# Optimization experiments

Hardware: AMD Instinct MI355X
Metric: run time of the kernel (lower is better)

## Reference

```python
import jax, jax.numpy as jnp
import numpy as np

D_MODEL = 2048
N_HEAD = 32
N_KV_HEAD = 8
HEAD_DIM = D_MODEL // N_HEAD  # 64
N_REP = N_HEAD // N_KV_HEAD   # 4
B, T = 2, 2048


def setup_inputs() -> dict:
    key = jax.random.key(0)
    ks = jax.random.split(key, 5)
    s = 0.02
    return {
        "x": jax.random.normal(ks[0], (B, T, D_MODEL), dtype=jnp.float32),
        "Wq": jax.random.normal(ks[1], (D_MODEL, N_HEAD * HEAD_DIM), dtype=jnp.float32) * s,
        "Wk": jax.random.normal(ks[2], (D_MODEL, N_KV_HEAD * HEAD_DIM), dtype=jnp.float32) * s,
        "Wv": jax.random.normal(ks[3], (D_MODEL, N_KV_HEAD * HEAD_DIM), dtype=jnp.float32) * s,
        "Wo": jax.random.normal(ks[4], (N_HEAD * HEAD_DIM, D_MODEL), dtype=jnp.float32) * s,
        "mask": 1,
    }


def _rope_tables(t_len, dim, dtype):
    inv_freq = 1.0 / (10000.0 ** (jnp.arange(0, dim, 2, dtype=jnp.float32) / dim))
    freqs = jnp.arange(t_len, dtype=jnp.float32)[:, None] * inv_freq[None, :]  # [T, dim/2]
    return jnp.cos(freqs).astype(dtype), jnp.sin(freqs).astype(dtype)


def _apply_rope(x, cos, sin):
    # x: [B, H, T, D]; cos/sin: [T, D/2]; half-concat layout as in source
    x1, x2 = x[..., ::2], x[..., 1::2]
    return jnp.concatenate([x1 * cos - x2 * sin, x1 * sin + x2 * cos], axis=-1)


def reference(x, Wq, Wk, Wv, Wo, mask):
    b, t, c = x.shape
    q = (x @ Wq).reshape(b, t, N_HEAD, HEAD_DIM).transpose(0, 2, 1, 3)      # [B,H,T,D]
    k = (x @ Wk).reshape(b, t, N_KV_HEAD, HEAD_DIM).transpose(0, 2, 1, 3)   # [B,Hkv,T,D]
    v = (x @ Wv).reshape(b, t, N_KV_HEAD, HEAD_DIM).transpose(0, 2, 1, 3)
    cos, sin = _rope_tables(t, HEAD_DIM, x.dtype)
    q = _apply_rope(q, cos, sin)
    k = _apply_rope(k, cos, sin)
    k = jnp.repeat(k, N_REP, axis=1)  # [B,H,T,D]
    v = jnp.repeat(v, N_REP, axis=1)
    scale = 1.0 / np.sqrt(HEAD_DIM)
    scores = jnp.einsum('bhtd,bhsd->bhts', q, k) * scale  # [B,H,T,T]
    if mask:
        causal = jnp.tril(jnp.ones((t, t), dtype=bool))
        scores = jnp.where(causal, scores, jnp.float32(-jnp.inf).astype(scores.dtype))
    weights = jax.nn.softmax(scores, axis=-1)
    out = jnp.einsum('bhts,bhsd->bhtd', weights, v)        # [B,H,T,D]
    out = out.transpose(0, 2, 1, 3).reshape(b, t, c)
    return out @ Wo
```

## Files before the change

### kernel.cpp

```cpp
#include <hip/hip_runtime.h>
#include <stdint.h>

#define D_MODEL 2048
#define N_HEAD 32
#define N_KV_HEAD 8
#define HEAD_DIM 64
#define BATCH 2
#define SEQ 2048
#define ROWS (BATCH*SEQ)
#define QKV_N 3072
#define SCL2F 0.18033688011112042f

typedef __attribute__((ext_vector_type(4))) float f32x4;
typedef __attribute__((ext_vector_type(8))) short bf16x8;

__device__ __forceinline__ float bflo(unsigned u){ return __uint_as_float(u << 16); }
__device__ __forceinline__ float bfhi(unsigned u){ return __uint_as_float(u & 0xFFFF0000u); }
__device__ __forceinline__ unsigned f2bf(float f){
  unsigned u = __float_as_uint(f);
  u += 0x7FFFu + ((u >> 16) & 1u);
  return u >> 16;
}
__device__ __forceinline__ unsigned cvtpk(float a, float b){
  unsigned r;
  asm("v_cvt_pk_bf16_f32 %0, %1, %2" : "=v"(r) : "v"(a), "v"(b));
  return r;
}

__device__ __forceinline__ void async_copy16(const void* g, void* lds){
  __builtin_amdgcn_global_load_lds(
      (const __attribute__((address_space(1))) void*)g,
      (__attribute__((address_space(3))) void*)lds, 16, 0, 0);
}

__global__ __launch_bounds__(256) void k_prep(const float* __restrict__ x,
                                              const float* __restrict__ Wq,
                                              const float* __restrict__ Wk,
                                              const float* __restrict__ Wv,
                                              const float* __restrict__ Wo,
                                              unsigned short* __restrict__ xb,
                                              unsigned short* __restrict__ Wqkvt,
                                              unsigned short* __restrict__ Wot,
                                              float* __restrict__ ct,
                                              float* __restrict__ st){
  __shared__ float tile[64][65];
  const int bid = blockIdx.x;
  const int tid = threadIdx.x;
  if (bid < 8192) {
    int i = bid*256 + tid;
    float4 v = ((const float4*)x)[i];
    unsigned lo = f2bf(v.x) | (f2bf(v.y) << 16);
    unsigned hi = f2bf(v.z) | (f2bf(v.w) << 16);
    ((uint2*)xb)[i] = make_uint2(lo, hi);
    return;
  }
  if (bid < 10752) {
    const int rel0 = bid - 8192;
    const float* W; unsigned short* Wt; int N; int rel;
    if (rel0 < 1024)      { W = Wq; Wt = Wqkvt;                         N = 2048; rel = rel0; }
    else if (rel0 < 1280) { W = Wk; Wt = Wqkvt + (size_t)2048*D_MODEL;  N = 512;  rel = rel0 - 1024; }
    else if (rel0 < 1536) { W = Wv; Wt = Wqkvt + (size_t)2560*D_MODEL;  N = 512;  rel = rel0 - 1280; }
    else                  { W = Wo; Wt = Wot;                           N = 2048; rel = rel0 - 1536; }
    const int ntn = N >> 6;
    const int tk = rel / ntn, tn = rel % ntn;
    #pragma unroll
    for (int i = 0; i < 4; ++i) {
      int idx4 = tid + 256*i;
      int r = idx4 >> 4;
      int c4 = idx4 & 15;
      float4 v = *(const float4*)(W + (size_t)(tk*64 + r)*N + tn*64 + c4*4);
      tile[r][c4*4+0] = v.x; tile[r][c4*4+1] = v.y;
      tile[r][c4*4+2] = v.z; tile[r][c4*4+3] = v.w;
    }
    __syncthreads();
    #pragma unroll
    for (int i = 0; i < 8; ++i) {
      int o2 = tid + 256*i;
      int n  = o2 >> 5;
      int k2 = o2 & 31;
      unsigned lo = f2bf(tile[k2*2+0][n]);
      unsigned hi = f2bf(tile[k2*2+1][n]);
      *(unsigned*)(Wt + (size_t)(tn*64 + n)*D_MODEL + tk*64 + k2*2) = lo | (hi << 16);
    }
    return;
  }
  {
    int gid = (bid - 10752)*256 + tid;
    int t = gid >> 5, d = gid & 31;
    float inv = exp2f(-13.287712379549449f * ((float)d * (1.0f/32.0f)));
    float a = (float)t * inv;
    ct[gid] = cosf(a);
    st[gid] = sinf(a);
  }
}

__global__ __launch_bounds__(256) void k_kv_prep(unsigned short* __restrict__ QKVb,
                                                 unsigned short* __restrict__ Vt,
                                                 const float* __restrict__ ct,
                                                 const float* __restrict__ st){
  __shared__ __align__(16) unsigned short tl[64*64];
  const int bid = blockIdx.x;
  const int tid = threadIdx.x;
  if (bid < 128) {
    int gid = bid*256 + tid;
    int row = gid >> 3;
    int h = gid & 7;
    int t = row & (SEQ-1);
    unsigned* p = (unsigned*)(QKVb + (size_t)row*QKV_N + 2048 + h*HEAD_DIM);
    float o1[32], o2[32];
    #pragma unroll
    for (int d = 0; d < 32; ++d) {
      unsigned u = p[d];
      float x1 = bflo(u), x2 = bfhi(u);
      float c = ct[t*32+d], s = st[t*32+d];
      o1[d] = x1*c - x2*s;
      o2[d] = x1*s + x2*c;
    }
    #pragma unroll
    for (int i = 0; i < 16; ++i) {
      p[i]    = f2bf(o1[2*i]) | (f2bf(o1[2*i+1]) << 16);
      p[16+i] = f2bf(o2[2*i]) | (f2bf(o2[2*i+1]) << 16);
    }
    return;
  }
  const int rel = bid - 128;
  const int bk = rel >> 5;
  const int stt = rel & 31;
  const int b = bk >> 3, kvh = bk & 7;
  #pragma unroll
  for (int it = 0; it < 2; ++it) {
    int i = tid + 256*it;
    int s = i >> 3, c = i & 7;
    uint4 v = *(const uint4*)(QKVb + (size_t)(b*SEQ + stt*64 + s)*QKV_N + 2560 + kvh*HEAD_DIM + c*8);
    *(uint4*)(tl + s*64 + ((c ^ (s&7))*8)) = v;
  }
  __syncthreads();
  const int d = tid & 63;
  const int w = tid >> 6;
  #pragma unroll
  for (int it = 0; it < 2; ++it) {
    int seg = w + it*4;
    unsigned short tmp[8];
    #pragma unroll
    for (int k = 0; k < 8; ++k) {
      int s = seg*8 + k;
      tmp[k] = tl[s*64 + (((d>>3) ^ (s&7))*8) + (d&7)];
    }
    *(uint4*)(Vt + ((size_t)bk*64 + d)*SEQ + stt*64 + seg*8) = *(uint4*)tmp;
  }
}

template<typename OUT_T>
__global__ __launch_bounds__(256) void k_gemm_bt(const unsigned short* __restrict__ A,
                                                 const unsigned short* __restrict__ Bt,
                                                 OUT_T* __restrict__ C,
                                                 int M, int N, int K){
  __shared__ unsigned short As[128*32];
  __shared__ unsigned short Bs[128*32];
  const int nbn = N >> 7;
  const int bswz = ((int)blockIdx.x & 7)*((int)gridDim.x >> 3) + ((int)blockIdx.x >> 3);
  const int bm = bswz / nbn, bn = bswz % nbn;
  const int m0 = bm << 7, n0 = bn << 7;
  const int tid = threadIdx.x;
  const int wid = tid >> 6, lane = tid & 63;
  const int wr = wid >> 1, wc = wid & 1;

  f32x4 acc[4][4] = {};

  const int ldr = lane >> 2;
  const int ldc = (lane & 3) * 8;
  const int fr  = lane & 15;
  const int fk  = (lane >> 4) * 8;

  for (int k0 = 0; k0 < K; k0 += 32) {
    #pragma unroll
    for (int i = 0; i < 2; ++i) {
      int chunk = wid*2 + i;
      int row = chunk*16 + ldr;
      async_copy16(A  + (size_t)(m0+row)*K + k0 + ldc, (void*)(As + chunk*512));
      async_copy16(Bt + (size_t)(n0+row)*K + k0 + ldc, (void*)(Bs + chunk*512));
    }
    __syncthreads();
    bf16x8 a[4], b[4];
    #pragma unroll
    for (int m = 0; m < 4; ++m) a[m] = *(const bf16x8*)(As + (wr*64 + m*16 + fr)*32 + fk);
    #pragma unroll
    for (int n = 0; n < 4; ++n) b[n] = *(const bf16x8*)(Bs + (wc*64 + n*16 + fr)*32 + fk);
    #pragma unroll
    for (int m = 0; m < 4; ++m)
      #pragma unroll
      for (int n = 0; n < 4; ++n)
        acc[m][n] = __builtin_amdgcn_mfma_f32_16x16x32_bf16(a[m], b[n], acc[m][n], 0, 0, 0);
    __syncthreads();
  }

  const int crow = (lane >> 4) * 4, ccol = lane & 15;
  #pragma unroll
  for (int m = 0; m < 4; ++m){
    #pragma unroll
    for (int n = 0; n < 4; ++n){
      size_t base = (size_t)(m0 + wr*64 + m*16 + crow)*N + (n0 + wc*64 + n*16 + ccol);
      #pragma unroll
      for (int j = 0; j < 4; ++j){
        float v = acc[m][n][j];
        if constexpr (sizeof(OUT_T) == 2)
          ((unsigned short*)C)[base + (size_t)j*N] = (unsigned short)f2bf(v);
        else
          ((float*)C)[base + (size_t)j*N] = v;
      }
    }
  }
}

__global__ __launch_bounds__(256) void k_attn_mfma(const unsigned short* __restrict__ Q,
                                                   const unsigned short* __restrict__ Kb,
                                                   const unsigned short* __restrict__ Vt,
                                                   unsigned short* __restrict__ O,
                                                   const int* __restrict__ maskp,
                                                   const float* __restrict__ ct,
                                                   const float* __restrict__ st){
  __shared__ __align__(16) char smem[40960];
  const int orig = blockIdx.x;
  const int bid = (orig & 7)*128 + (orig >> 3);
  const int jj = bid & 15;
  const int h  = (bid >> 4) & 31;
  const int b  = bid >> 9;
  const int kvh = h >> 2;
  const int tid = threadIdx.x;
  const int wid = tid >> 6, lane = tid & 63;
  const int q_ = lane & 15, g = lane >> 4;
  char* Psm = smem + 32768 + wid*2048;
  const bool causal = (maskp[0] != 0);

  bf16x8 onesf;
  #pragma unroll
  for (int e = 0; e < 8; ++e) onesf[e] = (short)0x3F80;

  auto stage = [&](int tile, int bufbase){
    const int s0s = tile*64;
    #pragma unroll
    for (int it = 0; it < 2; ++it) {
      int i = (wid*2+it)*64 + lane;
      int s = i >> 3, c = i & 7;
      async_copy16(Kb + (size_t)(b*SEQ + s0s + s)*QKV_N + kvh*HEAD_DIM + ((c ^ (s&7))*8),
                   smem + bufbase + (wid*2+it)*1024);
      async_copy16(Vt + ((size_t)(b*N_KV_HEAD + kvh)*HEAD_DIM + s)*SEQ + s0s + ((c ^ (s&7))*8),
                   smem + bufbase + 8192 + (wid*2+it)*1024);
    }
  };

  for (int pass = 0; pass < 2; ++pass) {
    const int qt = pass ? jj : (31 - jj);
    const int q0 = qt*64;
    const int qg = q0 + 16*wid + q_;
    const int nt = causal ? (qt+1) : (SEQ/64);

    bf16x8 qf0, qf1;
    {
      const int trow = qg;
      const unsigned short* qsrc = Q + (size_t)(b*SEQ + trow)*QKV_N + h*HEAD_DIM + g*16;
      union { bf16x8 h; unsigned u[4]; } xa, xb;
      xa.h = *(const bf16x8*)(qsrc);
      xb.h = *(const bf16x8*)(qsrc + 8);
      const float4* cp = (const float4*)(ct + trow*32 + g*8);
      const float4* sp = (const float4*)(st + trow*32 + g*8);
      float4 c0 = cp[0], c1 = cp[1];
      float4 s0 = sp[0], s1 = sp[1];
      float cc[8] = {c0.x,c0.y,c0.z,c0.w,c1.x,c1.y,c1.z,c1.w};
      float ss[8] = {s0.x,s0.y,s0.z,s0.w,s1.x,s1.y,s1.z,s1.w};
      float e0[8], e1[8];
      #pragma unroll
      for (int e = 0; e < 8; ++e) {
        unsigned u = (e < 4) ? xa.u[e] : xb.u[e-4];
        float x1 = bflo(u), x2 = bfhi(u);
        float cs = cc[e]*SCL2F, sn = ss[e]*SCL2F;
        e0[e] = x1*cs - x2*sn;
        e1[e] = x1*sn + x2*cs;
      }
      union { unsigned u[4]; bf16x8 h; } p0, p1;
      #pragma unroll
      for (int m = 0; m < 4; ++m) {
        p0.u[m] = cvtpk(e0[2*m], e0[2*m+1]);
        p1.u[m] = cvtpk(e1[2*m], e1[2*m+1]);
      }
      qf0 = p0.h; qf1 = p1.h;
    }

    f32x4 acc[4] = {};
    f32x4 accl = {};
    float mrun = -1e30f;

    __syncthreads();
    stage(0, 0);

    for (int t = 0; t < nt; ++t) {
      const int s0 = t*64;
      const int cur = t & 1;

      asm volatile("s_waitcnt vmcnt(0)" ::: "memory");
      __syncthreads();
      if (t+1 < nt) stage(t+1, (cur^1)*16384);

      const char* Kbuf = smem + cur*16384;
      const char* Vbuf = Kbuf + 8192;

      f32x4 sa[4];
      __builtin_amdgcn_s_setprio(1);
      #pragma unroll
      for (int f = 0; f < 4; ++f) {
        const char* kb = Kbuf + (16*f + q_)*128;
        bf16x8 a0 = *(const bf16x8*)(kb + ((g ^ (q_&7))*16));
        bf16x8 a1 = *(const bf16x8*)(kb + (((g+4) ^ (q_&7))*16));
        f32x4 z = {};
        z = __builtin_amdgcn_mfma_f32_16x16x32_bf16(a0, qf0, z, 0, 0, 0);
        z = __builtin_amdgcn_mfma_f32_16x16x32_bf16(a1, qf1, z, 0, 0, 0);
        sa[f] = z;
      }
      __builtin_amdgcn_s_setprio(0);

      const bool domask = causal && (t == qt);
      float x[4][4];
      float cm[4];
      #pragma unroll
      for (int f = 0; f < 4; ++f) {
        #pragma unroll
        for (int r = 0; r < 4; ++r) {
          float v = sa[f][r];
          if (domask && (s0 + 16*f + 4*g + r > qg)) v = -3.0e38f;
          x[f][r] = v;
        }
        cm[f] = fmaxf(fmaxf(x[f][0], x[f][1]), fmaxf(x[f][2], x[f][3]));
      }
      float cmax = fmaxf(fmaxf(cm[0], cm[1]), fmaxf(cm[2], cm[3]));
      cmax = fmaxf(cmax, __shfl_xor(cmax, 16));
      cmax = fmaxf(cmax, __shfl_xor(cmax, 32));
      if (!__all(cmax <= mrun + 8.0f)) {
        float mnew = fmaxf(mrun, cmax);
        float r2 = exp2f(mrun - mnew);
        #pragma unroll
        for (int m = 0; m < 4; ++m) {
          acc[m][0] *= r2; acc[m][1] *= r2; acc[m][2] *= r2; acc[m][3] *= r2;
        }
        accl[0] *= r2; accl[1] *= r2; accl[2] *= r2; accl[3] *= r2;
        mrun = mnew;
      }
      #pragma unroll
      for (int f = 0; f < 4; ++f) {
        float e0 = exp2f(x[f][0] - mrun);
        float e1 = exp2f(x[f][1] - mrun);
        float e2 = exp2f(x[f][2] - mrun);
        float e3 = exp2f(x[f][3] - mrun);
        uint2 w = { cvtpk(e0, e1), cvtpk(e2, e3) };
        int byteo = q_*128 + (((2*f + (g>>1)) ^ (q_&7))*16) + (g&1)*8;
        *(uint2*)(Psm + byteo) = w;
      }

      __builtin_amdgcn_s_setprio(1);
      #pragma unroll
      for (int kh = 0; kh < 2; ++kh) {
        bf16x8 pb = *(const bf16x8*)(Psm + q_*128 + (((g + 4*kh) ^ (q_&7))*16));
        accl = __builtin_amdgcn_mfma_f32_16x16x32_bf16(onesf, pb, accl, 0, 0, 0);
        #pragma unroll
        for (int m = 0; m < 4; ++m) {
          bf16x8 va = *(const bf16x8*)(Vbuf + (16*m + q_)*128 + (((g + 4*kh) ^ (q_&7))*16));
          acc[m] = __builtin_amdgcn_mfma_f32_16x16x32_bf16(va, pb, acc[m], 0, 0, 0);
        }
      }
      __builtin_amdgcn_s_setprio(0);
    }

    float inv = 1.0f / accl[0];
    #pragma unroll
    for (int m = 0; m < 4; ++m) {
      uint2 w = { cvtpk(acc[m][0]*inv, acc[m][1]*inv), cvtpk(acc[m][2]*inv, acc[m][3]*inv) };
      int byteo = q_*128 + (((2*m + (g>>1)) ^ (q_&7))*16) + (g&1)*8;
      *(uint2*)(Psm + byteo) = w;
    }
    #pragma unroll
    for (int cc = 0; cc < 2; ++cc) {
      int row = lane >> 2;
      int ch = (lane & 3)*2 + cc;
      uint4 v = *(const uint4*)(Psm + row*128 + ((ch ^ (row&7))*16));
      *(uint4*)(O + (size_t)(b*SEQ + q0 + 16*wid + row)*D_MODEL + h*HEAD_DIM + ch*8) = v;
    }
  }
}

extern "C" void kernel_launch(void* const* d_in, const int* in_sizes, int n_in,
                              void* d_out, int out_size, void* d_ws, size_t ws_size,
                              hipStream_t stream){
  const float* x  = (const float*)d_in[0];
  const float* Wq = (const float*)d_in[1];
  const float* Wk = (const float*)d_in[2];
  const float* Wv = (const float*)d_in[3];
  const float* Wo = (const float*)d_in[4];
  const int* maskp = (const int*)d_in[5];
  float* out = (float*)d_out;

  char* ws = (char*)d_ws;
  unsigned short* xb    = (unsigned short*)(ws);
  unsigned short* AO    = (unsigned short*)(ws);
  unsigned short* Wqkvt = (unsigned short*)(ws + 16777216);
  unsigned short* Vt    = (unsigned short*)(ws + 16777216);
  unsigned short* Wot   = (unsigned short*)(ws + 29360128);
  unsigned short* QKVb  = (unsigned short*)(ws + 37748736);
  float* ct = (float*)(ws + 62914560);
  float* st = (float*)(ws + 63176704);

  k_prep<<<11008, 256, 0, stream>>>(x, Wq, Wk, Wv, Wo, xb, Wqkvt, Wot, ct, st);

  k_gemm_bt<unsigned short><<<(4096/128)*(QKV_N/128), 256, 0, stream>>>(xb, Wqkvt, QKVb, 4096, QKV_N, 2048);

  k_kv_prep<<<1152, 256, 0, stream>>>(QKVb, Vt, ct, st);

  k_attn_mfma<<<BATCH*N_HEAD*16, 256, 0, stream>>>(QKVb, QKVb + 2048, Vt, AO, maskp, ct, st);

  k_gemm_bt<float><<<(4096/128)*(2048/128), 256, 0, stream>>>(AO, Wot, out, 4096, 2048, 2048);
}
```

Measured before the change: 241.4 us.

## Split attention softmax into two independent half-tile streams with separate running max

Each 64-key tile is processed as two 32-key halves that keep independent running maxima, denominators and output accumulators, and the two are merged only at the end. The first half's exp and PV MFMAs can then overlap with the second half's max reduction, shortening the serial dependency chain per tile. Global staging pointers are precomputed and advanced by fixed strides, and the launch bounds now request 4 blocks per CU. In exchange, the doubled accumulators raise register pressure, which could cause spills or clash with the occupancy target.

```diff
diff --git a/kernel.cpp b/kernel.cpp
--- a/kernel.cpp
+++ b/kernel.cpp
@@ -212,13 +212,13 @@
   }
 }
 
-__global__ __launch_bounds__(256) void k_attn_mfma(const unsigned short* __restrict__ Q,
-                                                   const unsigned short* __restrict__ Kb,
-                                                   const unsigned short* __restrict__ Vt,
-                                                   unsigned short* __restrict__ O,
-                                                   const int* __restrict__ maskp,
-                                                   const float* __restrict__ ct,
-                                                   const float* __restrict__ st){
+__global__ __launch_bounds__(256, 4) void k_attn_mfma(const unsigned short* __restrict__ Q,
+                                                      const unsigned short* __restrict__ Kb,
+                                                      const unsigned short* __restrict__ Vt,
+                                                      unsigned short* __restrict__ O,
+                                                      const int* __restrict__ maskp,
+                                                      const float* __restrict__ ct,
+                                                      const float* __restrict__ st){
   __shared__ __align__(16) char smem[40960];
   const int orig = blockIdx.x;
   const int bid = (orig & 7)*128 + (orig >> 3);
@@ -236,18 +236,10 @@
   #pragma unroll
   for (int e = 0; e < 8; ++e) onesf[e] = (short)0x3F80;
 
-  auto stage = [&](int tile, int bufbase){
-    const int s0s = tile*64;
-    #pragma unroll
-    for (int it = 0; it < 2; ++it) {
-      int i = (wid*2+it)*64 + lane;
-      int s = i >> 3, c = i & 7;
-      async_copy16(Kb + (size_t)(b*SEQ + s0s + s)*QKV_N + kvh*HEAD_DIM + ((c ^ (s&7))*8),
-                   smem + bufbase + (wid*2+it)*1024);
-      async_copy16(Vt + ((size_t)(b*N_KV_HEAD + kvh)*HEAD_DIM + s)*SEQ + s0s + ((c ^ (s&7))*8),
-                   smem + bufbase + 8192 + (wid*2+it)*1024);
-    }
-  };
+  const int i0 = (wid*2+0)*64 + lane, sA_ = i0 >> 3, cA_ = i0 & 7;
+  const int i1 = (wid*2+1)*64 + lane, sB_ = i1 >> 3, cB_ = i1 & 7;
+  const size_t KADV = (size_t)64*QKV_N*sizeof(unsigned short);
+  const size_t VADV = (size_t)64*sizeof(unsigned short);
 
   for (int pass = 0; pass < 2; ++pass) {
     const int qt = pass ? jj : (31 - jj);
@@ -265,9 +257,9 @@
       const float4* cp = (const float4*)(ct + trow*32 + g*8);
       const float4* sp = (const float4*)(st + trow*32 + g*8);
       float4 c0 = cp[0], c1 = cp[1];
-      float4 s0 = sp[0], s1 = sp[1];
+      float4 s0v = sp[0], s1v = sp[1];
       float cc[8] = {c0.x,c0.y,c0.z,c0.w,c1.x,c1.y,c1.z,c1.w};
-      float ss[8] = {s0.x,s0.y,s0.z,s0.w,s1.x,s1.y,s1.z,s1.w};
+      float ss[8] = {s0v.x,s0v.y,s0v.z,s0v.w,s1v.x,s1v.y,s1v.z,s1v.w};
       float e0[8], e1[8];
       #pragma unroll
       for (int e = 0; e < 8; ++e) {
@@ -286,12 +278,25 @@
       qf0 = p0.h; qf1 = p1.h;
     }
 
-    f32x4 acc[4] = {};
-    f32x4 accl = {};
-    float mrun = -1e30f;
+    f32x4 accA[4] = {}, accB[4] = {};
+    f32x4 acclA = {}, acclB = {};
+    float mA = -1e30f, mB = -1e30f;
+
+    const char* kp0 = (const char*)(Kb + (size_t)(b*SEQ + sA_)*QKV_N + kvh*HEAD_DIM + ((cA_^(sA_&7))*8));
+    const char* kp1 = (const char*)(Kb + (size_t)(b*SEQ + sB_)*QKV_N + kvh*HEAD_DIM + ((cB_^(sB_&7))*8));
+    const char* vp0 = (const char*)(Vt + ((size_t)(b*N_KV_HEAD + kvh)*HEAD_DIM + sA_)*SEQ + ((cA_^(sA_&7))*8));
+    const char* vp1 = (const char*)(Vt + ((size_t)(b*N_KV_HEAD + kvh)*HEAD_DIM + sB_)*SEQ + ((cB_^(sB_&7))*8));
+
+    auto stage = [&](int bufbase){
+      async_copy16(kp0, smem + bufbase + (wid*2+0)*1024);
+      async_copy16(kp1, smem + bufbase + (wid*2+1)*1024);
+      async_copy16(vp0, smem + bufbase + 8192 + (wid*2+0)*1024);
+      async_copy16(vp1, smem + bufbase + 8192 + (wid*2+1)*1024);
+      kp0 += KADV; kp1 += KADV; vp0 += VADV; vp1 += VADV;
+    };
 
     __syncthreads();
-    stage(0, 0);
+    stage(0);
 
     for (int t = 0; t < nt; ++t) {
       const int s0 = t*64;
@@ -299,7 +304,7 @@
 
       asm volatile("s_waitcnt vmcnt(0)" ::: "memory");
       __syncthreads();
-      if (t+1 < nt) stage(t+1, (cur^1)*16384);
+      if (t+1 < nt) stage((cur^1)*16384);
 
       const char* Kbuf = smem + cur*16384;
       const char* Vbuf = Kbuf + 8192;
@@ -319,60 +324,104 @@
       __builtin_amdgcn_s_setprio(0);
 
       const bool domask = causal && (t == qt);
-      float x[4][4];
-      float cm[4];
-      #pragma unroll
-      for (int f = 0; f < 4; ++f) {
-        #pragma unroll
-        for (int r = 0; r < 4; ++r) {
-          float v = sa[f][r];
-          if (domask && (s0 + 16*f + 4*g + r > qg)) v = -3.0e38f;
-          x[f][r] = v;
-        }
-        cm[f] = fmaxf(fmaxf(x[f][0], x[f][1]), fmaxf(x[f][2], x[f][3]));
-      }
-      float cmax = fmaxf(fmaxf(cm[0], cm[1]), fmaxf(cm[2], cm[3]));
-      cmax = fmaxf(cmax, __shfl_xor(cmax, 16));
-      cmax = fmaxf(cmax, __shfl_xor(cmax, 32));
-      if (!__all(cmax <= mrun + 8.0f)) {
-        float mnew = fmaxf(mrun, cmax);
-        float r2 = exp2f(mrun - mnew);
+
+      {
+        #pragma unroll
+        for (int f = 0; f < 2; ++f)
+          #pragma unroll
+          for (int r = 0; r < 4; ++r)
+            if (domask && (s0 + 16*f + 4*g + r > qg)) sa[f][r] = -3.0e38f;
+        float c0 = fmaxf(fmaxf(sa[0][0], sa[0][1]), fmaxf(sa[0][2], sa[0][3]));
+        float c1 = fmaxf(fmaxf(sa[1][0], sa[1][1]), fmaxf(sa[1][2], sa[1][3]));
+        float cmax = fmaxf(c0, c1);
+        cmax = fmaxf(cmax, __shfl_xor(cmax, 16));
+        cmax = fmaxf(cmax, __shfl_xor(cmax, 32));
+        if (!__all(cmax <= mA + 8.0f)) {
+          float mnew = fmaxf(mA, cmax);
+          float r2 = exp2f(mA - mnew);
+          #pragma unroll
+          for (int m = 0; m < 4; ++m) {
+            accA[m][0] *= r2; accA[m][1] *= r2; accA[m][2] *= r2; accA[m][3] *= r2;
+          }
+          acclA[0] *= r2; acclA[1] *= r2; acclA[2] *= r2; acclA[3] *= r2;
+          mA = mnew;
+        }
+        #pragma unroll
+        for (int f = 0; f < 2; ++f) {
+          float e0 = exp2f(sa[f][0] - mA);
+          float e1 = exp2f(sa[f][1] - mA);
+          float e2 = exp2f(sa[f][2] - mA);
+          float e3 = exp2f(sa[f][3] - mA);
+          uint2 w = { cvtpk(e0, e1), cvtpk(e2, e3) };
+          int byteo = q_*128 + (((2*f + (g>>1)) ^ (q_&7))*16) + (g&1)*8;
+          *(uint2*)(Psm + byteo) = w;
+        }
+        __builtin_amdgcn_s_setprio(1);
+        bf16x8 pb = *(const bf16x8*)(Psm + q_*128 + ((g ^ (q_&7))*16));
+        acclA = __builtin_amdgcn_mfma_f32_16x16x32_bf16(onesf, pb, acclA, 0, 0, 0);
         #pragma unroll
         for (int m = 0; m < 4; ++m) {
-          acc[m][0] *= r2; acc[m][1] *= r2; acc[m][2] *= r2; acc[m][3] *= r2;
-        }
-        accl[0] *= r2; accl[1] *= r2; accl[2] *= r2; accl[3] *= r2;
-        mrun = mnew;
-      }
-      #pragma unroll
-      for (int f = 0; f < 4; ++f) {
-        float e0 = exp2f(x[f][0] - mrun);
-        float e1 = exp2f(x[f][1] - mrun);
-        float e2 = exp2f(x[f][2] - mrun);
-        float e3 = exp2f(x[f][3] - mrun);
-        uint2 w = { cvtpk(e0, e1), cvtpk(e2, e3) };
-        int byteo = q_*128 + (((2*f + (g>>1)) ^ (q_&7))*16) + (g&1)*8;
-        *(uint2*)(Psm + byteo) = w;
-      }
-
-      __builtin_amdgcn_s_setprio(1);
-      #pragma unroll
-      for (int kh = 0; kh < 2; ++kh) {
-        bf16x8 pb = *(const bf16x8*)(Psm + q_*128 + (((g + 4*kh) ^ (q_&7))*16));
-        accl = __builtin_amdgcn_mfma_f32_16x16x32_bf16(onesf, pb, accl, 0, 0, 0);
+          bf16x8 va = *(const bf16x8*)(Vbuf + (16*m + q_)*128 + ((g ^ (q_&7))*16));
+          accA[m] = __builtin_amdgcn_mfma_f32_16x16x32_bf16(va, pb, accA[m], 0, 0, 0);
+        }
+        __builtin_amdgcn_s_setprio(0);
+      }
+
+      {
+        #pragma unroll
+        for (int f = 2; f < 4; ++f)
+          #pragma unroll
+          for (int r = 0; r < 4; ++r)
+            if (domask && (s0 + 16*f + 4*g + r > qg)) sa[f][r] = -3.0e38f;
+        float c0 = fmaxf(fmaxf(sa[2][0], sa[2][1]), fmaxf(sa[2][2], sa[2][3]));
+        float c1 = fmaxf(fmaxf(sa[3][0], sa[3][1]), fmaxf(sa[3][2], sa[3][3]));
+        float cmax = fmaxf(c0, c1);
+        cmax = fmaxf(cmax, __shfl_xor(cmax, 16));
+        cmax = fmaxf(cmax, __shfl_xor(cmax, 32));
+        if (!__all(cmax <= mB + 8.0f)) {
+          float mnew = fmaxf(mB, cmax);
+          float r2 = exp2f(mB - mnew);
+          #pragma unroll
+          for (int m = 0; m < 4; ++m) {
+            accB[m][0] *= r2; accB[m][1] *= r2; accB[m][2] *= r2; accB[m][3] *= r2;
+          }
+          acclB[0] *= r2; acclB[1] *= r2; acclB[2] *= r2; acclB[3] *= r2;
+          mB = mnew;
+        }
+        #pragma unroll
+        for (int f = 2; f < 4; ++f) {
+          float e0 = exp2f(sa[f][0] - mB);
+          float e1 = exp2f(sa[f][1] - mB);
+          float e2 = exp2f(sa[f][2] - mB);
+          float e3 = exp2f(sa[f][3] - mB);
+          uint2 w = { cvtpk(e0, e1), cvtpk(e2, e3) };
+          int byteo = q_*128 + (((2*f + (g>>1)) ^ (q_&7))*16) + (g&1)*8;
+          *(uint2*)(Psm + byteo) = w;
+        }
+        __builtin_amdgcn_s_setprio(1);
+        bf16x8 pb = *(const bf16x8*)(Psm + q_*128 + (((g + 4) ^ (q_&7))*16));
+        acclB = __builtin_amdgcn_mfma_f32_16x16x32_bf16(onesf, pb, acclB, 0, 0, 0);
         #pragma unroll
         for (int m = 0; m < 4; ++m) {
-          bf16x8 va = *(const bf16x8*)(Vbuf + (16*m + q_)*128 + (((g + 4*kh) ^ (q_&7))*16));
-          acc[m] = __builtin_amdgcn_mfma_f32_16x16x32_bf16(va, pb, acc[m], 0, 0, 0);
-        }
-      }
-      __builtin_amdgcn_s_setprio(0);
-    }
-
-    float inv = 1.0f / accl[0];
+          bf16x8 va = *(const bf16x8*)(Vbuf + (16*m + q_)*128 + (((g + 4) ^ (q_&7))*16));
+          accB[m] = __builtin_amdgcn_mfma_f32_16x16x32_bf16(va, pb, accB[m], 0, 0, 0);
+        }
+        __builtin_amdgcn_s_setprio(0);
+      }
+    }
+
+    float mm = fmaxf(mA, mB);
+    float rA = exp2f(mA - mm), rB = exp2f(mB - mm);
+    float denom = acclA[0]*rA + acclB[0]*rB;
+    float invd = 1.0f / denom;
+    rA *= invd; rB *= invd;
     #pragma unroll
     for (int m = 0; m < 4; ++m) {
-      uint2 w = { cvtpk(acc[m][0]*inv, acc[m][1]*inv), cvtpk(acc[m][2]*inv, acc[m][3]*inv) };
+      float o0 = accA[m][0]*rA + accB[m][0]*rB;
+      float o1 = accA[m][1]*rA + accB[m][1]*rB;
+      float o2 = accA[m][2]*rA + accB[m][2]*rB;
+      float o3 = accA[m][3]*rA + accB[m][3]*rB;
+      uint2 w = { cvtpk(o0, o1), cvtpk(o2, o3) };
       int byteo = q_*128 + (((2*m + (g>>1)) ^ (q_&7))*16) + (g&1)*8;
       *(uint2*)(Psm + byteo) = w;
     }
```

Measured after the change: 244.3 us. Within noise of the previous version (+1.2%).

## Replace GEMM with 256-wide 8-wave pipelined kernel and split attention K/V staging

Applied to the files above, without the earlier changes.

Swaps the simple 128x128 single-buffered GEMM for a templated 512-thread kernel. It uses 256-wide N tiles, 64-wide K steps with double buffering, XOR-swizzled LDS and interleaved phases that keep async copies in flight under the MFMAs. The attention kernel now double-buffers only K and single-buffers V, which cuts LDS use, and loads the next V tile after the PV step. Both changes aim to hide global memory latency and raise MFMA use. The cost is heavy reliance on hand-tuned vmcnt counts and barriers, plus a grid of only 192–256 blocks, which may not fill every CU.

```diff
diff --git a/kernel.cpp b/kernel.cpp
--- a/kernel.cpp
+++ b/kernel.cpp
@@ -150,56 +150,111 @@
   }
 }
 
-template<typename OUT_T>
-__global__ __launch_bounds__(256) void k_gemm_bt(const unsigned short* __restrict__ A,
-                                                 const unsigned short* __restrict__ Bt,
-                                                 OUT_T* __restrict__ C,
-                                                 int M, int N, int K){
-  __shared__ unsigned short As[128*32];
-  __shared__ unsigned short Bs[128*32];
-  const int nbn = N >> 7;
+template<int MREP, typename OUT_T>
+__global__ __launch_bounds__(512, 1) void k_gemm8(const unsigned short* __restrict__ A,
+                                                  const unsigned short* __restrict__ Bt,
+                                                  OUT_T* __restrict__ C,
+                                                  int M, int N, int K){
+  constexpr int BM = MREP*32;
+  constexpr int ABYTES = BM*128;
+  constexpr int AHALF  = BM*64;
+  constexpr int BUF = ABYTES + 32768;
+  constexpr int LA = MREP/4;
+  constexpr int VMW = 6 + 2*LA;
+
+  __shared__ __align__(16) char smem[2*BUF];
+
+  const int nbn = N >> 8;
   const int bswz = ((int)blockIdx.x & 7)*((int)gridDim.x >> 3) + ((int)blockIdx.x >> 3);
-  const int bm = bswz / nbn, bn = bswz % nbn;
-  const int m0 = bm << 7, n0 = bn << 7;
+  const int m0 = (bswz / nbn) * BM;
+  const int n0 = (bswz % nbn) * 256;
   const int tid = threadIdx.x;
   const int wid = tid >> 6, lane = tid & 63;
-  const int wr = wid >> 1, wc = wid & 1;
-
-  f32x4 acc[4][4] = {};
-
-  const int ldr = lane >> 2;
-  const int ldc = (lane & 3) * 8;
-  const int fr  = lane & 15;
-  const int fk  = (lane >> 4) * 8;
-
-  for (int k0 = 0; k0 < K; k0 += 32) {
-    #pragma unroll
-    for (int i = 0; i < 2; ++i) {
-      int chunk = wid*2 + i;
-      int row = chunk*16 + ldr;
-      async_copy16(A  + (size_t)(m0+row)*K + k0 + ldc, (void*)(As + chunk*512));
-      async_copy16(Bt + (size_t)(n0+row)*K + k0 + ldc, (void*)(Bs + chunk*512));
-    }
-    __syncthreads();
-    bf16x8 a[4], b[4];
-    #pragma unroll
-    for (int m = 0; m < 4; ++m) a[m] = *(const bf16x8*)(As + (wr*64 + m*16 + fr)*32 + fk);
-    #pragma unroll
-    for (int n = 0; n < 4; ++n) b[n] = *(const bf16x8*)(Bs + (wc*64 + n*16 + fr)*32 + fk);
-    #pragma unroll
-    for (int m = 0; m < 4; ++m)
-      #pragma unroll
-      for (int n = 0; n < 4; ++n)
-        acc[m][n] = __builtin_amdgcn_mfma_f32_16x16x32_bf16(a[m], b[n], acc[m][n], 0, 0, 0);
-    __syncthreads();
-  }
-
-  const int crow = (lane >> 4) * 4, ccol = lane & 15;
+  const int wm = wid >> 2, wn = wid & 3;
+  const int fr = lane & 15, q = lane >> 4;
+  const int NT = K >> 6;
+  const int NITER = NT >> 1;
+  const size_t rb = (size_t)K*2;
+
+  f32x4 acc[MREP][4] = {};
+  bf16x8 Bfrag[4];
+
+  const int srow = tid >> 2, sq = tid & 3;
+
+  auto stageA = [&](int t, int ks, int bufb){
+    #pragma unroll
+    for (int r = 0; r < LA; ++r){
+      int row = r*128 + srow;
+      int sw = ((row >> 1) & 3);
+      async_copy16((const char*)A + (size_t)(m0+row)*rb + t*128 + ks*64 + ((sq ^ sw)*16),
+                   smem + bufb + ks*AHALF + (r*512 + tid)*16);
+    }
+  };
+  auto stageB = [&](int t, int ks, int bufb){
+    #pragma unroll
+    for (int r = 0; r < 2; ++r){
+      int row = r*128 + srow;
+      int sw = ((row >> 1) & 3);
+      async_copy16((const char*)Bt + (size_t)(n0+row)*rb + t*128 + ks*64 + ((sq ^ sw)*16),
+                   smem + bufb + ABYTES + ks*16384 + (r*512 + tid)*16);
+    }
+  };
+
+#define PHASE(KS, MH, BUFB, LOADB, STAGE_STMT, DO_VMCNT) {                              \
+    bf16x8 Af[MREP/2];                                                                  \
+    _Pragma("unroll")                                                                   \
+    for (int mm = 0; mm < MREP/2; ++mm){                                                \
+      int row = wm*(MREP*16) + ((MH)*(MREP/2)+mm)*16 + fr;                              \
+      Af[mm] = *(const bf16x8*)(smem + (BUFB) + (KS)*AHALF + row*64 +                   \
+                                ((q ^ ((row>>1)&3))*16));                               \
+    }                                                                                   \
+    if (LOADB){                                                                         \
+      _Pragma("unroll")                                                                 \
+      for (int n = 0; n < 4; ++n){                                                      \
+        int row = wn*64 + n*16 + fr;                                                    \
+        Bfrag[n] = *(const bf16x8*)(smem + (BUFB) + ABYTES + (KS)*16384 + row*64 +      \
+                                    ((q ^ ((row>>1)&3))*16));                           \
+      }                                                                                 \
+    }                                                                                   \
+    STAGE_STMT;                                                                         \
+    __builtin_amdgcn_s_barrier();                                                       \
+    __builtin_amdgcn_s_setprio(1);                                                      \
+    _Pragma("unroll")                                                                   \
+    for (int mm = 0; mm < MREP/2; ++mm)                                                 \
+      _Pragma("unroll")                                                                 \
+      for (int n = 0; n < 4; ++n)                                                       \
+        acc[(MH)*(MREP/2)+mm][n] = __builtin_amdgcn_mfma_f32_16x16x32_bf16(             \
+            Af[mm], Bfrag[n], acc[(MH)*(MREP/2)+mm][n], 0, 0, 0);                       \
+    __builtin_amdgcn_s_setprio(0);                                                      \
+    if (DO_VMCNT) asm volatile("s_waitcnt vmcnt(%0)" :: "n"(VMW) : "memory");           \
+    __builtin_amdgcn_s_barrier();                                                       \
+  }
+
+  stageB(0, 0, 0);  stageA(0, 0, 0);  stageB(0, 1, 0);  stageA(0, 1, 0);
+  stageB(1, 0, BUF); stageA(1, 0, BUF); stageB(1, 1, BUF);
+  asm volatile("s_waitcnt vmcnt(%0)" :: "n"(VMW) : "memory");
+  __builtin_amdgcn_s_barrier();
+
+  for (int i = 0; i < NITER; ++i){
+    const int t2 = (2*i+2) & (NT-1);
+    const int t3 = (2*i+3) & (NT-1);
+    PHASE(0, 0, 0,   true,  stageA(2*i+1, 1, BUF), false)
+    PHASE(0, 1, 0,   false, stageB(t2, 0, 0),      true)
+    PHASE(1, 0, 0,   true,  stageA(t2, 0, 0),      false)
+    PHASE(1, 1, 0,   false, stageB(t2, 1, 0),      true)
+    PHASE(0, 0, BUF, true,  stageA(t2, 1, 0),      false)
+    PHASE(0, 1, BUF, false, stageB(t3, 0, BUF),    true)
+    PHASE(1, 0, BUF, true,  stageA(t3, 0, BUF),    false)
+    PHASE(1, 1, BUF, false, stageB(t3, 1, BUF),    true)
+  }
+#undef PHASE
+
+  asm volatile("s_waitcnt vmcnt(0)" ::: "memory");
   #pragma unroll
-  for (int m = 0; m < 4; ++m){
+  for (int m = 0; m < MREP; ++m){
     #pragma unroll
     for (int n = 0; n < 4; ++n){
-      size_t base = (size_t)(m0 + wr*64 + m*16 + crow)*N + (n0 + wc*64 + n*16 + ccol);
+      size_t base = (size_t)(m0 + wm*(MREP*16) + m*16 + q*4)*N + (n0 + wn*64 + n*16 + fr);
       #pragma unroll
       for (int j = 0; j < 4; ++j){
         float v = acc[m][n][j];
@@ -219,7 +274,8 @@
                                                    const int* __restrict__ maskp,
                                                    const float* __restrict__ ct,
                                                    const float* __restrict__ st){
-  __shared__ __align__(16) char smem[40960];
+  __shared__ __align__(16) char smem[32768];
+  char* Vsm = smem + 16384;
   const int orig = blockIdx.x;
   const int bid = (orig & 7)*128 + (orig >> 3);
   const int jj = bid & 15;
@@ -229,14 +285,14 @@
   const int tid = threadIdx.x;
   const int wid = tid >> 6, lane = tid & 63;
   const int q_ = lane & 15, g = lane >> 4;
-  char* Psm = smem + 32768 + wid*2048;
+  char* Psm = smem + 24576 + wid*2048;
   const bool causal = (maskp[0] != 0);
 
   bf16x8 onesf;
   #pragma unroll
   for (int e = 0; e < 8; ++e) onesf[e] = (short)0x3F80;
 
-  auto stage = [&](int tile, int bufbase){
+  auto stageK = [&](int tile, int bufbase){
     const int s0s = tile*64;
     #pragma unroll
     for (int it = 0; it < 2; ++it) {
@@ -244,8 +300,16 @@
       int s = i >> 3, c = i & 7;
       async_copy16(Kb + (size_t)(b*SEQ + s0s + s)*QKV_N + kvh*HEAD_DIM + ((c ^ (s&7))*8),
                    smem + bufbase + (wid*2+it)*1024);
+    }
+  };
+  auto stageV = [&](int tile){
+    const int s0s = tile*64;
+    #pragma unroll
+    for (int it = 0; it < 2; ++it) {
+      int i = (wid*2+it)*64 + lane;
+      int s = i >> 3, c = i & 7;
       async_copy16(Vt + ((size_t)(b*N_KV_HEAD + kvh)*HEAD_DIM + s)*SEQ + s0s + ((c ^ (s&7))*8),
-                   smem + bufbase + 8192 + (wid*2+it)*1024);
+                   Vsm + (wid*2+it)*1024);
     }
   };
 
@@ -290,19 +354,17 @@
     f32x4 accl = {};
     float mrun = -1e30f;
 
+    stageK(0, 0);
+    stageV(0);
+    asm volatile("s_waitcnt vmcnt(0)" ::: "memory");
     __syncthreads();
-    stage(0, 0);
 
     for (int t = 0; t < nt; ++t) {
       const int s0 = t*64;
       const int cur = t & 1;
-
-      asm volatile("s_waitcnt vmcnt(0)" ::: "memory");
-      __syncthreads();
-      if (t+1 < nt) stage(t+1, (cur^1)*16384);
-
-      const char* Kbuf = smem + cur*16384;
-      const char* Vbuf = Kbuf + 8192;
+      const char* Kbuf = smem + cur*8192;
+
+      if (t+1 < nt) stageK(t+1, (cur^1)*8192);
 
       f32x4 sa[4];
       __builtin_amdgcn_s_setprio(1);
@@ -355,6 +417,9 @@
         *(uint2*)(Psm + byteo) = w;
       }
 
+      asm volatile("s_waitcnt vmcnt(0)" ::: "memory");
+      __syncthreads();
+
       __builtin_amdgcn_s_setprio(1);
       #pragma unroll
       for (int kh = 0; kh < 2; ++kh) {
@@ -362,11 +427,14 @@
         accl = __builtin_amdgcn_mfma_f32_16x16x32_bf16(onesf, pb, accl, 0, 0, 0);
         #pragma unroll
         for (int m = 0; m < 4; ++m) {
-          bf16x8 va = *(const bf16x8*)(Vbuf + (16*m + q_)*128 + (((g + 4*kh) ^ (q_&7))*16));
+          bf16x8 va = *(const bf16x8*)(Vsm + (16*m + q_)*128 + (((g + 4*kh) ^ (q_&7))*16));
           acc[m] = __builtin_amdgcn_mfma_f32_16x16x32_bf16(va, pb, acc[m], 0, 0, 0);
         }
       }
       __builtin_amdgcn_s_setprio(0);
+
+      __syncthreads();
+      if (t+1 < nt) stageV(t+1);
     }
 
     float inv = 1.0f / accl[0];
@@ -409,11 +477,11 @@
 
   k_prep<<<11008, 256, 0, stream>>>(x, Wq, Wk, Wv, Wo, xb, Wqkvt, Wot, ct, st);
 
-  k_gemm_bt<unsigned short><<<(4096/128)*(QKV_N/128), 256, 0, stream>>>(xb, Wqkvt, QKVb, 4096, QKV_N, 2048);
+  k_gemm8<8, unsigned short><<<192, 512, 0, stream>>>(xb, Wqkvt, QKVb, 4096, QKV_N, 2048);
 
   k_kv_prep<<<1152, 256, 0, stream>>>(QKVb, Vt, ct, st);
 
   k_attn_mfma<<<BATCH*N_HEAD*16, 256, 0, stream>>>(QKVb, QKVb + 2048, Vt, AO, maskp, ct, st);
 
-  k_gemm_bt<float><<<(4096/128)*(2048/128), 256, 0, stream>>>(AO, Wot, out, 4096, 2048, 2048);
-}
+  k_gemm8<4, float><<<256, 512, 0, stream>>>(AO, Wot, out, 4096, 2048, 2048);
+}
```

Measured after the change: 208.3 us. -13.7%, faster.
